# Kernel tuning notes

Measured on AMD Instinct MI355X. Metric: run time of the kernel, lower is better.

Reference implementation:

```python
import jax, jax.numpy as jnp
import numpy as np

N = 50000          # total nodes (types: 20000/17000/13000)
E = 800000         # edges, avg degree 16
NUM_ETYPES = 6
ALPHA = 0.05       # residual-attention blend coefficient
SLOPE = 0.2        # leaky_relu negative slope


def _edge_softmax(e, dst, n):
    # softmax over incoming edges of each destination node; e: [E, H]
    m = jax.ops.segment_max(e, dst, num_segments=n)      # [N, H]
    ex = jnp.exp(e - m[dst])
    s = jax.ops.segment_sum(ex, dst, num_segments=n)     # [N, H]
    return ex / s[dst]


def _gat_layer(h, src, dst, etype, W, We, eemb, al, ar, ae, resW, res_attn, activate):
    n = h.shape[0]
    H, out = al.shape
    feat = (h @ W).reshape(n, H, out)                    # [N, H, out]
    T, edim = eemb.shape
    # edge-type attention term: embedding -> fc_e -> attn_e; only T distinct rows
    et_att = jnp.einsum('thd,hd->th', (eemb @ We).reshape(T, H, edim), ae)  # [T, H]
    el = jnp.einsum('nho,ho->nh', feat, al)              # [N, H]
    er = jnp.einsum('nho,ho->nh', feat, ar)              # [N, H]
    e = jax.nn.leaky_relu(el[src] + er[dst] + et_att[etype], SLOPE)  # [E, H]
    a = _edge_softmax(e, dst, n)                         # [E, H]
    if res_attn is not None:
        a = a * (1.0 - ALPHA) + res_attn * ALPHA
    rst = jax.ops.segment_sum(feat[src] * a[:, :, None], dst, num_segments=n)  # [N, H, out]
    if resW is not None:
        rst = rst + (h @ resW).reshape(n, H, out)
    if activate:
        rst = jax.nn.elu(rst)
    return rst, jax.lax.stop_gradient(a)


def _forward(x0, x1, x2, fcw0, fcb0, fcw1, fcb1, fcw2, fcb2,
             W0, We0, eemb0, al0, ar0, ae0,
             W1, We1, eemb1, al1, ar1, ae1, resW1,
             W2, We2, eemb2, al2, ar2, ae2, resW2,
             src, dst, etype):
    # per-type input projection then concat (feat_drop=0 -> identity)
    h = jnp.concatenate([x0 @ fcw0 + fcb0, x1 @ fcw1 + fcb1, x2 @ fcw2 + fcb2], axis=0)  # [N, 64]
    h1, a = _gat_layer(h, src, dst, etype, W0, We0, eemb0, al0, ar0, ae0, None, None, True)
    h1 = h1.reshape(h1.shape[0], -1)                     # [N, 256]
    h2, a = _gat_layer(h1, src, dst, etype, W1, We1, eemb1, al1, ar1, ae1, resW1, a, True)
    h2 = h2.reshape(h2.shape[0], -1)                     # [N, 256]
    logits, _ = _gat_layer(h2, src, dst, etype, W2, We2, eemb2, al2, ar2, ae2, resW2, None, False)
    return logits                                        # [N, 1, 16]


def setup_inputs():
    key = jax.random.key(0)
    ks = iter(jax.random.split(key, 48))
    def rn(shape, fan_in):
        return jax.random.normal(next(ks), shape, jnp.float32) / np.sqrt(fan_in)
    inp = {}
    inp['x0'] = jax.random.normal(next(ks), (20000, 128), jnp.float32)
    inp['x1'] = jax.random.normal(next(ks), (17000, 256), jnp.float32)
    inp['x2'] = jax.random.normal(next(ks), (13000, 64), jnp.float32)
    inp['fcw0'] = rn((128, 64), 128); inp['fcb0'] = jnp.zeros((64,), jnp.float32)
    inp['fcw1'] = rn((256, 64), 256); inp['fcb1'] = jnp.zeros((64,), jnp.float32)
    inp['fcw2'] = rn((64, 64), 64);   inp['fcb2'] = jnp.zeros((64,), jnp.float32)
    # layer 0: in=64 -> H=8, out=32
    inp['W0'] = rn((64, 256), 64); inp['We0'] = rn((64, 512), 64)
    inp['eemb0'] = rn((NUM_ETYPES, 64), 1.0)
    inp['al0'] = rn((8, 32), 32); inp['ar0'] = rn((8, 32), 32); inp['ae0'] = rn((8, 64), 64)
    # layer 1: in=256 -> H=8, out=32, residual
    inp['W1'] = rn((256, 256), 256); inp['We1'] = rn((64, 512), 64)
    inp['eemb1'] = rn((NUM_ETYPES, 64), 1.0)
    inp['al1'] = rn((8, 32), 32); inp['ar1'] = rn((8, 32), 32); inp['ae1'] = rn((8, 64), 64)
    inp['resW1'] = rn((256, 256), 256)
    # output layer: in=256 -> H=1, out=16, residual
    inp['W2'] = rn((256, 16), 256); inp['We2'] = rn((64, 64), 64)
    inp['eemb2'] = rn((NUM_ETYPES, 64), 1.0)
    inp['al2'] = rn((1, 16), 16); inp['ar2'] = rn((1, 16), 16); inp['ae2'] = rn((1, 64), 64)
    inp['resW2'] = rn((256, 16), 256)
    inp['src'] = jax.random.randint(next(ks), (E,), 0, N)
    inp['dst'] = jax.random.randint(next(ks), (E,), 0, N)
    inp['etype'] = jax.random.randint(next(ks), (E,), 0, NUM_ETYPES)
    return inp


def reference(x0, x1, x2, fcw0, fcb0, fcw1, fcb1, fcw2, fcb2,
              W0, We0, eemb0, al0, ar0, ae0,
              W1, We1, eemb1, al1, ar1, ae1, resW1,
              W2, We2, eemb2, al2, ar2, ae2, resW2,
              src, dst, etype):
    return _forward(x0, x1, x2, fcw0, fcb0, fcw1, fcb1, fcw2, fcb2,
                    W0, We0, eemb0, al0, ar0, ae0,
                    W1, We1, eemb1, al1, ar1, ae1, resW1,
                    W2, We2, eemb2, al2, ar2, ae2, resW2,
                    src, dst, etype)
```

## Files before the change

kernel.cpp:

```cpp
#include <hip/hip_runtime.h>
#include <hip/hip_bf16.h>

#define ALPHA 0.05f
#define SLOPE 0.2f
#define LCAP 128

typedef __attribute__((ext_vector_type(8))) short short8v;
typedef __attribute__((ext_vector_type(8))) unsigned short ushort8v;
typedef __attribute__((ext_vector_type(4))) float floatx4;

__device__ inline ushort f2b(float f) {
    uint u = __float_as_uint(f);
    return (ushort)((u + 0x7fffu + ((u >> 16) & 1u)) >> 16);
}
__device__ inline float b2f(ushort b) { return __uint_as_float(((uint)b) << 16); }

__device__ inline void gload_lds16(const ushort* g, ushort* l) {
    __builtin_amdgcn_global_load_lds(
        (const __attribute__((address_space(1))) uint*)g,
        (__attribute__((address_space(3))) uint*)l, 16, 0, 0);
}


__global__ void hist_kernel(const int* __restrict__ dst, int* __restrict__ counts, int E) {
    int e = blockIdx.x * blockDim.x + threadIdx.x;
    if (e < E) atomicAdd(&counts[dst[e]], 1);
}

__global__ __launch_bounds__(256) void scan_part(const int* __restrict__ counts,
                                                 int* __restrict__ offsets,
                                                 int* __restrict__ partial, int n) {
    __shared__ int sd[256];
    int i = blockIdx.x * 256 + threadIdx.x;
    int v = (i < n) ? counts[i] : 0;
    sd[threadIdx.x] = v;
    __syncthreads();
    for (int off = 1; off < 256; off <<= 1) {
        int t = (threadIdx.x >= off) ? sd[threadIdx.x - off] : 0;
        __syncthreads();
        sd[threadIdx.x] += t;
        __syncthreads();
    }
    if (i < n) offsets[i + 1] = sd[threadIdx.x];
    if (threadIdx.x == 255) partial[blockIdx.x] = sd[255];
}

__global__ __launch_bounds__(256) void scan_top(int* __restrict__ partial, int nb) {
    __shared__ int sd[256];
    int v = (threadIdx.x < nb) ? partial[threadIdx.x] : 0;
    sd[threadIdx.x] = v;
    __syncthreads();
    for (int off = 1; off < 256; off <<= 1) {
        int t = (threadIdx.x >= off) ? sd[threadIdx.x - off] : 0;
        __syncthreads();
        sd[threadIdx.x] += t;
        __syncthreads();
    }
    if (threadIdx.x < nb) partial[threadIdx.x] = sd[threadIdx.x];
}

__global__ __launch_bounds__(256) void scan_add(int* __restrict__ offsets,
                                                int* __restrict__ cursor,
                                                const int* __restrict__ partial, int n) {
    int i = blockIdx.x * 256 + threadIdx.x;
    if (i >= n) return;
    int add = (blockIdx.x > 0) ? partial[blockIdx.x - 1] : 0;
    int v = offsets[i + 1] + add;
    offsets[i + 1] = v;
    if (i + 1 < n) cursor[i + 1] = v;
    if (i == 0) { offsets[0] = 0; cursor[0] = 0; }
}

__global__ void scatter_kernel(const int* __restrict__ src, const int* __restrict__ dst,
                               const int* __restrict__ et, int* __restrict__ cursor,
                               int* __restrict__ se, int E) {
    int e = blockIdx.x * blockDim.x + threadIdx.x;
    if (e >= E) return;
    int d = dst[e];
    int pos = atomicAdd(&cursor[d], 1);
    se[pos] = (src[e] << 3) | et[e];
}


__global__ void wprep(const float* __restrict__ W0f, const float* __restrict__ W1f,
                      const float* __restrict__ WRf,
                      const float* __restrict__ fw0, const float* __restrict__ fw1,
                      const float* __restrict__ fw2,
                      const float* __restrict__ W2f, const float* __restrict__ WR2f,
                      ushort* __restrict__ Wt0, ushort* __restrict__ Wt1,
                      ushort* __restrict__ WtR,
                      ushort* __restrict__ ft0, ushort* __restrict__ ft1,
                      ushort* __restrict__ ft2, ushort* __restrict__ Wt2R) {
    int i = blockIdx.x * blockDim.x + threadIdx.x;
    if (i < 16384) {
        int k = i / 256, n = i % 256;
        Wt0[n * 64 + k] = f2b(W0f[i]);
    } else if (i < 16384 + 65536) {
        int j = i - 16384;
        int k = j / 256, n = j % 256;
        Wt1[n * 256 + k] = f2b(W1f[j]);
    } else if (i < 16384 + 2 * 65536) {
        int j = i - 16384 - 65536;
        int k = j / 256, n = j % 256;
        WtR[n * 256 + k] = f2b(WRf[j]);
    } else if (i < 147456 + 8192) {
        int j = i - 147456;
        int k = j / 64, n = j % 64;
        ft0[n * 128 + k] = f2b(fw0[j]);
    } else if (i < 147456 + 8192 + 16384) {
        int j = i - 147456 - 8192;
        int k = j / 64, n = j % 64;
        ft1[n * 256 + k] = f2b(fw1[j]);
    } else if (i < 147456 + 8192 + 16384 + 4096) {
        int j = i - 147456 - 8192 - 16384;
        int k = j / 64, n = j % 64;
        ft2[n * 64 + k] = f2b(fw2[j]);
    } else if (i < 176128 + 4096) {
        int j = i - 176128;
        int k = j / 16, n = j % 16;
        Wt2R[n * 256 + k] = f2b(W2f[j]);
    } else if (i < 176128 + 8192) {
        int j = i - 176128 - 4096;
        int k = j / 16, n = j % 16;
        Wt2R[(16 + n) * 256 + k] = f2b(WR2f[j]);
    }
}


__global__ __launch_bounds__(512) void etype_all(
    const float* __restrict__ eemb0, const float* __restrict__ We0, const float* __restrict__ ae0, float* __restrict__ out0,
    const float* __restrict__ eemb1, const float* __restrict__ We1, const float* __restrict__ ae1, float* __restrict__ out1,
    const float* __restrict__ eemb2, const float* __restrict__ We2, const float* __restrict__ ae2, float* __restrict__ out2) {
    int layer = blockIdx.x / 6, t = blockIdx.x % 6;
    const float *eemb, *We, *ae;
    float* out;
    int H;
    if (layer == 0)      { eemb = eemb0; We = We0; ae = ae0; out = out0; H = 8; }
    else if (layer == 1) { eemb = eemb1; We = We1; ae = ae1; out = out1; H = 8; }
    else                 { eemb = eemb2; We = We2; ae = ae2; out = out2; H = 1; }
    __shared__ float es[64];
    int j = threadIdx.x;
    if (j < 64) es[j] = eemb[t * 64 + j];
    __syncthreads();
    if (j >= H * 64) return;
    float wsum = 0.f;
#pragma unroll 8
    for (int k = 0; k < 64; ++k) wsum += es[k] * We[k * (H * 64) + j];
    float v = wsum * ae[j];
#pragma unroll
    for (int off = 32; off > 0; off >>= 1) v += __shfl_down(v, off, 64);
    if ((j & 63) == 0) out[t * H + (j >> 6)] = v;
}


template<bool ATTN>
__global__ __launch_bounds__(256) void gemm_bf16(const ushort* __restrict__ A,
                                                 const ushort* __restrict__ Bt,
                                                 ushort* __restrict__ Cb,
                                                 const float* __restrict__ al,
                                                 const float* __restrict__ ar,
                                                 float* __restrict__ el,
                                                 float* __restrict__ er,
                                                 int M, int N, int K) {
    __shared__ ushort As[128 * 32];
    __shared__ ushort Bs[128 * 32];
    int bm = blockIdx.y * 128, bn = blockIdx.x * 128;
    int tid = threadIdx.x;
    int wave = tid >> 6, lane = tid & 63;
    int wm = (wave >> 1) * 64, wn = (wave & 1) * 64;
    int r = tid >> 2, c = (tid & 3) * 8;
    floatx4 acc[4][4] = {};
    for (int k0 = 0; k0 < K; k0 += 32) {
        gload_lds16(&A[(long)(bm + r) * K + k0 + c],       &As[(size_t)tid * 8]);
        gload_lds16(&A[(long)(bm + 64 + r) * K + k0 + c],  &As[(size_t)(256 + tid) * 8]);
        gload_lds16(&Bt[(long)(bn + r) * K + k0 + c],      &Bs[(size_t)tid * 8]);
        gload_lds16(&Bt[(long)(bn + 64 + r) * K + k0 + c], &Bs[(size_t)(256 + tid) * 8]);
        __syncthreads();
        int lr = lane & 15, lk = (lane >> 4) * 8;
        short8v af[4], bfr[4];
#pragma unroll
        for (int i = 0; i < 4; ++i)
            af[i] = *reinterpret_cast<const short8v*>(&As[(wm + i * 16 + lr) * 32 + lk]);
#pragma unroll
        for (int j = 0; j < 4; ++j)
            bfr[j] = *reinterpret_cast<const short8v*>(&Bs[(wn + j * 16 + lr) * 32 + lk]);
#pragma unroll
        for (int i = 0; i < 4; ++i)
#pragma unroll
            for (int j = 0; j < 4; ++j)
                acc[i][j] = __builtin_amdgcn_mfma_f32_16x16x32_bf16(af[i], bfr[j], acc[i][j], 0, 0, 0);
        __syncthreads();
    }
    int col = lane & 15, rbase = (lane >> 4) * 4;
#pragma unroll
    for (int i = 0; i < 4; ++i) {
#pragma unroll
        for (int rr = 0; rr < 4; ++rr) {
            int gm = bm + wm + i * 16 + rbase + rr;
            if (gm >= M) continue;
#pragma unroll
            for (int j = 0; j < 4; ++j) {
                int gn = bn + wn + j * 16 + col;
                Cb[(long)gm * N + gn] = f2b(acc[i][j][rr]);
            }
        }
    }
    if (ATTN) {
        int hA = (bn + wn) >> 5;
        float alv[4], arv[4];
#pragma unroll
        for (int j = 0; j < 4; ++j) {
            int h = hA + (j >> 1);
            int o = (j & 1) * 16 + col;
            alv[j] = al[h * 32 + o];
            arv[j] = ar[h * 32 + o];
        }
#pragma unroll
        for (int i = 0; i < 4; ++i) {
#pragma unroll
            for (int rr = 0; rr < 4; ++rr) {
                float slA = acc[i][0][rr] * alv[0] + acc[i][1][rr] * alv[1];
                float slB = acc[i][2][rr] * alv[2] + acc[i][3][rr] * alv[3];
                float srA = acc[i][0][rr] * arv[0] + acc[i][1][rr] * arv[1];
                float srB = acc[i][2][rr] * arv[2] + acc[i][3][rr] * arv[3];
#pragma unroll
                for (int off = 1; off < 16; off <<= 1) {
                    slA += __shfl_xor(slA, off, 64);
                    slB += __shfl_xor(slB, off, 64);
                    srA += __shfl_xor(srA, off, 64);
                    srB += __shfl_xor(srB, off, 64);
                }
                int gm = bm + wm + i * 16 + rbase + rr;
                if (col == 0 && gm < M) {
                    el[gm * 8 + hA]     = slA;
                    el[gm * 8 + hA + 1] = slB;
                    er[gm * 8 + hA]     = srA;
                    er[gm * 8 + hA + 1] = srB;
                }
            }
        }
    }
}


__global__ __launch_bounds__(256) void gemm_dual(const ushort* __restrict__ A,
                                                 const ushort* __restrict__ B1,
                                                 const ushort* __restrict__ B2,
                                                 ushort* __restrict__ C1,
                                                 ushort* __restrict__ C2,
                                                 const float* __restrict__ al,
                                                 const float* __restrict__ ar,
                                                 float* __restrict__ el,
                                                 float* __restrict__ er,
                                                 int M, int N, int K) {
    __shared__ ushort As[128 * 32];
    __shared__ ushort Bs1[128 * 32];
    __shared__ ushort Bs2[128 * 32];
    int bm = blockIdx.y * 128, bn = blockIdx.x * 128;
    int tid = threadIdx.x;
    int wave = tid >> 6, lane = tid & 63;
    int wm = (wave >> 1) * 64, wn = (wave & 1) * 64;
    int r = tid >> 2, c = (tid & 3) * 8;
    floatx4 acc1[4][4] = {};
    floatx4 acc2[4][4] = {};
    for (int k0 = 0; k0 < K; k0 += 32) {
        gload_lds16(&A[(long)(bm + r) * K + k0 + c],        &As[(size_t)tid * 8]);
        gload_lds16(&A[(long)(bm + 64 + r) * K + k0 + c],   &As[(size_t)(256 + tid) * 8]);
        gload_lds16(&B1[(long)(bn + r) * K + k0 + c],       &Bs1[(size_t)tid * 8]);
        gload_lds16(&B1[(long)(bn + 64 + r) * K + k0 + c],  &Bs1[(size_t)(256 + tid) * 8]);
        gload_lds16(&B2[(long)(bn + r) * K + k0 + c],       &Bs2[(size_t)tid * 8]);
        gload_lds16(&B2[(long)(bn + 64 + r) * K + k0 + c],  &Bs2[(size_t)(256 + tid) * 8]);
        __syncthreads();
        int lr = lane & 15, lk = (lane >> 4) * 8;
        short8v af[4], bfr[4];
#pragma unroll
        for (int i = 0; i < 4; ++i)
            af[i] = *reinterpret_cast<const short8v*>(&As[(wm + i * 16 + lr) * 32 + lk]);
#pragma unroll
        for (int j = 0; j < 4; ++j)
            bfr[j] = *reinterpret_cast<const short8v*>(&Bs1[(wn + j * 16 + lr) * 32 + lk]);
#pragma unroll
        for (int i = 0; i < 4; ++i)
#pragma unroll
            for (int j = 0; j < 4; ++j)
                acc1[i][j] = __builtin_amdgcn_mfma_f32_16x16x32_bf16(af[i], bfr[j], acc1[i][j], 0, 0, 0);
#pragma unroll
        for (int j = 0; j < 4; ++j)
            bfr[j] = *reinterpret_cast<const short8v*>(&Bs2[(wn + j * 16 + lr) * 32 + lk]);
#pragma unroll
        for (int i = 0; i < 4; ++i)
#pragma unroll
            for (int j = 0; j < 4; ++j)
                acc2[i][j] = __builtin_amdgcn_mfma_f32_16x16x32_bf16(af[i], bfr[j], acc2[i][j], 0, 0, 0);
        __syncthreads();
    }
    int col = lane & 15, rbase = (lane >> 4) * 4;
#pragma unroll
    for (int i = 0; i < 4; ++i) {
#pragma unroll
        for (int rr = 0; rr < 4; ++rr) {
            int gm = bm + wm + i * 16 + rbase + rr;
            if (gm >= M) continue;
#pragma unroll
            for (int j = 0; j < 4; ++j) {
                int gn = bn + wn + j * 16 + col;
                C1[(long)gm * N + gn] = f2b(acc1[i][j][rr]);
                C2[(long)gm * N + gn] = f2b(acc2[i][j][rr]);
            }
        }
    }
    int hA = (bn + wn) >> 5;
    float alv[4], arv[4];
#pragma unroll
    for (int j = 0; j < 4; ++j) {
        int h = hA + (j >> 1);
        int o = (j & 1) * 16 + col;
        alv[j] = al[h * 32 + o];
        arv[j] = ar[h * 32 + o];
    }
#pragma unroll
    for (int i = 0; i < 4; ++i) {
#pragma unroll
        for (int rr = 0; rr < 4; ++rr) {
            float slA = acc1[i][0][rr] * alv[0] + acc1[i][1][rr] * alv[1];
            float slB = acc1[i][2][rr] * alv[2] + acc1[i][3][rr] * alv[3];
            float srA = acc1[i][0][rr] * arv[0] + acc1[i][1][rr] * arv[1];
            float srB = acc1[i][2][rr] * arv[2] + acc1[i][3][rr] * arv[3];
#pragma unroll
            for (int off = 1; off < 16; off <<= 1) {
                slA += __shfl_xor(slA, off, 64);
                slB += __shfl_xor(slB, off, 64);
                srA += __shfl_xor(srA, off, 64);
                srB += __shfl_xor(srB, off, 64);
            }
            int gm = bm + wm + i * 16 + rbase + rr;
            if (col == 0 && gm < M) {
                el[gm * 8 + hA]     = slA;
                el[gm * 8 + hA + 1] = slB;
                er[gm * 8 + hA]     = srA;
                er[gm * 8 + hA + 1] = srB;
            }
        }
    }
}


__global__ __launch_bounds__(256) void gemm_fc(const float* __restrict__ x0,
                                               const float* __restrict__ x1,
                                               const float* __restrict__ x2,
                                               const ushort* __restrict__ ft0,
                                               const ushort* __restrict__ ft1,
                                               const ushort* __restrict__ ft2,
                                               const float* __restrict__ b0,
                                               const float* __restrict__ b1,
                                               const float* __restrict__ b2,
                                               ushort* __restrict__ C,
                                               int n0, int n1, int n2) {
    int z = blockIdx.z;
    const float* A;
    const ushort* Bt;
    const float* bias;
    int M, K;
    long coff;
    if (z == 0)      { A = x0; Bt = ft0; bias = b0; M = n0; K = 128; coff = 0; }
    else if (z == 1) { A = x1; Bt = ft1; bias = b1; M = n1; K = 256; coff = (long)n0 * 64; }
    else             { A = x2; Bt = ft2; bias = b2; M = n2; K = 64;  coff = (long)(n0 + n1) * 64; }
    int bm = blockIdx.y * 128;
    if (bm >= M) return;
    __shared__ ushort As[128 * 32];
    __shared__ ushort Bs[64 * 32];
    int tid = threadIdx.x;
    int wave = tid >> 6, lane = tid & 63;
    int wm = (wave >> 1) * 64, wn = (wave & 1) * 32;
    int r = tid >> 2, c = (tid & 3) * 8;
    floatx4 acc[4][2] = {};
    for (int k0 = 0; k0 < K; k0 += 32) {
        {
            int gm0 = bm + r, gm1 = bm + 64 + r;
            ushort8v u0 = {0, 0, 0, 0, 0, 0, 0, 0};
            ushort8v u1 = {0, 0, 0, 0, 0, 0, 0, 0};
            if (gm0 < M) {
                float4 lo = *reinterpret_cast<const float4*>(&A[(long)gm0 * K + k0 + c]);
                float4 hi = *reinterpret_cast<const float4*>(&A[(long)gm0 * K + k0 + c + 4]);
                u0[0] = f2b(lo.x); u0[1] = f2b(lo.y); u0[2] = f2b(lo.z); u0[3] = f2b(lo.w);
                u0[4] = f2b(hi.x); u0[5] = f2b(hi.y); u0[6] = f2b(hi.z); u0[7] = f2b(hi.w);
            }
            if (gm1 < M) {
                float4 lo = *reinterpret_cast<const float4*>(&A[(long)gm1 * K + k0 + c]);
                float4 hi = *reinterpret_cast<const float4*>(&A[(long)gm1 * K + k0 + c + 4]);
                u1[0] = f2b(lo.x); u1[1] = f2b(lo.y); u1[2] = f2b(lo.z); u1[3] = f2b(lo.w);
                u1[4] = f2b(hi.x); u1[5] = f2b(hi.y); u1[6] = f2b(hi.z); u1[7] = f2b(hi.w);
            }
            *reinterpret_cast<ushort8v*>(&As[(size_t)tid * 8]) = u0;
            *reinterpret_cast<ushort8v*>(&As[(size_t)(256 + tid) * 8]) = u1;
        }
        gload_lds16(&Bt[(long)r * K + k0 + c], &Bs[(size_t)tid * 8]);
        __syncthreads();
        int lr = lane & 15, lk = (lane >> 4) * 8;
        short8v af[4], bfr[2];
#pragma unroll
        for (int i = 0; i < 4; ++i)
            af[i] = *reinterpret_cast<const short8v*>(&As[(wm + i * 16 + lr) * 32 + lk]);
#pragma unroll
        for (int j = 0; j < 2; ++j)
            bfr[j] = *reinterpret_cast<const short8v*>(&Bs[(wn + j * 16 + lr) * 32 + lk]);
#pragma unroll
        for (int i = 0; i < 4; ++i)
#pragma unroll
            for (int j = 0; j < 2; ++j)
                acc[i][j] = __builtin_amdgcn_mfma_f32_16x16x32_bf16(af[i], bfr[j], acc[i][j], 0, 0, 0);
        __syncthreads();
    }
    int col = lane & 15, rbase = (lane >> 4) * 4;
#pragma unroll
    for (int i = 0; i < 4; ++i) {
#pragma unroll
        for (int rr = 0; rr < 4; ++rr) {
            int gm = bm + wm + i * 16 + rbase + rr;
            if (gm >= M) continue;
#pragma unroll
            for (int j = 0; j < 2; ++j) {
                int gn = wn + j * 16 + col;
                C[coff + (long)gm * 64 + gn] = f2b(acc[i][j][rr] + bias[gn]);
            }
        }
    }
}


__global__ __launch_bounds__(256) void gemm_small(const ushort* __restrict__ A,
                                                  const ushort* __restrict__ Wt2R,
                                                  ushort* __restrict__ feat2b,
                                                  float* __restrict__ resout,
                                                  const float* __restrict__ al,
                                                  const float* __restrict__ ar,
                                                  float* __restrict__ el,
                                                  float* __restrict__ er, int M) {
    __shared__ ushort As[128 * 32];
    __shared__ ushort Bs[32 * 256];
    int tid = threadIdx.x;
    int wave = tid >> 6, lane = tid & 63;
    int bm = blockIdx.x * 128;
    for (int i = tid; i < 32 * 256 / 8; i += 256)
        *reinterpret_cast<ushort8v*>(&Bs[(size_t)i * 8]) =
            *reinterpret_cast<const ushort8v*>(&Wt2R[(size_t)i * 8]);
    __syncthreads();
    int r = tid >> 2, c = (tid & 3) * 8;
    floatx4 acc[2][2] = {};
    for (int k0 = 0; k0 < 256; k0 += 32) {
        gload_lds16(&A[(long)(bm + r) * 256 + k0 + c],      &As[(size_t)tid * 8]);
        gload_lds16(&A[(long)(bm + 64 + r) * 256 + k0 + c], &As[(size_t)(256 + tid) * 8]);
        __syncthreads();
        int lr = lane & 15, lk = (lane >> 4) * 8;
        short8v af[2], bfr[2];
#pragma unroll
        for (int i = 0; i < 2; ++i)
            af[i] = *reinterpret_cast<const short8v*>(&As[(wave * 32 + i * 16 + lr) * 32 + lk]);
#pragma unroll
        for (int j = 0; j < 2; ++j)
            bfr[j] = *reinterpret_cast<const short8v*>(&Bs[(j * 16 + lr) * 256 + k0 + lk]);
#pragma unroll
        for (int i = 0; i < 2; ++i)
#pragma unroll
            for (int j = 0; j < 2; ++j)
                acc[i][j] = __builtin_amdgcn_mfma_f32_16x16x32_bf16(af[i], bfr[j], acc[i][j], 0, 0, 0);
        __syncthreads();
    }
    int col = lane & 15, rbase = (lane >> 4) * 4;
    float alv = al[col], arv = ar[col];
#pragma unroll
    for (int i = 0; i < 2; ++i) {
#pragma unroll
        for (int rr = 0; rr < 4; ++rr) {
            int gm = bm + wave * 32 + i * 16 + rbase + rr;
            float s1 = acc[i][0][rr];
            float s2 = acc[i][1][rr];
            float sl = s1 * alv, sr = s1 * arv;
#pragma unroll
            for (int off = 1; off < 16; off <<= 1) {
                sl += __shfl_xor(sl, off, 64);
                sr += __shfl_xor(sr, off, 64);
            }
            if (gm < M) {
                feat2b[(long)gm * 16 + col] = f2b(s1);
                resout[(long)gm * 16 + col] = s2;
                if (col == 0) { el[gm] = sl; er[gm] = sr; }
            }
        }
    }
}


template<bool BLEND, bool SAVE, bool RES>
__global__ __launch_bounds__(64) void fused_edge_h8(
    const int* __restrict__ offsets, const int* __restrict__ se,
    const float* __restrict__ el, const float* __restrict__ er,
    const float* __restrict__ etatt,
    const ushort* __restrict__ featb,
    const ushort* __restrict__ a0_in, ushort* __restrict__ a0_out,
    const ushort* __restrict__ resin, ushort* __restrict__ outb, int N) {
    int d = blockIdx.x;
    int lane = threadIdx.x;
    int lo = offsets[d], hi = offsets[d + 1];
    int deg = hi - lo;
    __shared__ float a_lds[LCAP][8];
    __shared__ int   s_lds[LCAP];
    __shared__ float er_s[8];
    __shared__ float m_s[8], inv_s[8];
    if (lane < 8) er_s[lane] = er[d * 8 + lane];
    __syncthreads();
    bool fast = (deg <= LCAP);
    int half = lane >> 5, t = lane & 31;
    int h8 = t >> 2;
    uint4 pf[4];
    int npf = 0;
    if (fast) {
        for (int i = lane; i < deg * 8; i += 64) {
            int p = i >> 3, h = i & 7;
            int v0 = se[lo + p];
            int s = v0 >> 3, tt = v0 & 7;
            if (h == 0) s_lds[p] = s;
            float v = el[s * 8 + h] + er_s[h] + etatt[tt * 8 + h];
            a_lds[p][h] = v > 0.f ? v : SLOPE * v;
        }
        __syncthreads();
#pragma unroll
        for (int u = 0; u < 4; ++u) {
            int p = half + 2 * u;
            if (p < deg) {
                pf[u] = *reinterpret_cast<const uint4*>(&featb[(long)s_lds[p] * 256 + t * 8]);
                npf = u + 1;
            }
        }
        {
            int g = lane >> 3, h = lane & 7;
            float m = -INFINITY;
            for (int p = g; p < deg; p += 8) m = fmaxf(m, a_lds[p][h]);
#pragma unroll
            for (int off = 8; off < 64; off <<= 1) m = fmaxf(m, __shfl_xor(m, off, 64));
            float ssum = 0.f;
            for (int p = g; p < deg; p += 8) ssum += __expf(a_lds[p][h] - m);
#pragma unroll
            for (int off = 8; off < 64; off <<= 1) ssum += __shfl_xor(ssum, off, 64);
            if (g == 0) {
                m_s[h] = m;
                inv_s[h] = ssum > 0.f ? 1.f / ssum : 0.f;
            }
        }
        __syncthreads();
        for (int i = lane; i < deg * 8; i += 64) {
            int p = i >> 3, h = i & 7;
            float a = __expf(a_lds[p][h] - m_s[h]) * inv_s[h];
            if (BLEND) a = a * (1.f - ALPHA) + b2f(a0_in[lo * 8 + i]) * ALPHA;
            a_lds[p][h] = a;
            if (SAVE) a0_out[lo * 8 + i] = f2b(a);
        }
        __syncthreads();
    } else {
        int g = lane >> 3, h = lane & 7;
        float m = -INFINITY;
        for (int p = g; p < deg; p += 8) {
            int v0 = se[lo + p];
            int s = v0 >> 3, tt = v0 & 7;
            float v = el[s * 8 + h] + er_s[h] + etatt[tt * 8 + h];
            v = v > 0.f ? v : SLOPE * v;
            m = fmaxf(m, v);
        }
#pragma unroll
        for (int off = 8; off < 64; off <<= 1) m = fmaxf(m, __shfl_xor(m, off, 64));
        float ssum = 0.f;
        for (int p = g; p < deg; p += 8) {
            int v0 = se[lo + p];
            int s = v0 >> 3, tt = v0 & 7;
            float v = el[s * 8 + h] + er_s[h] + etatt[tt * 8 + h];
            v = v > 0.f ? v : SLOPE * v;
            ssum += __expf(v - m);
        }
#pragma unroll
        for (int off = 8; off < 64; off <<= 1) ssum += __shfl_xor(ssum, off, 64);
        if (g == 0) {
            m_s[h] = m;
            inv_s[h] = ssum > 0.f ? 1.f / ssum : 0.f;
        }
        __syncthreads();
        if (SAVE) {
            for (int i = lane; i < deg * 8; i += 64) {
                int p = i >> 3, hh = i & 7;
                int v0 = se[lo + p];
                int s = v0 >> 3, tt = v0 & 7;
                float v = el[s * 8 + hh] + er_s[hh] + etatt[tt * 8 + hh];
                v = v > 0.f ? v : SLOPE * v;
                float a = __expf(v - m_s[hh]) * inv_s[hh];
                if (BLEND) a = a * (1.f - ALPHA) + b2f(a0_in[lo * 8 + i]) * ALPHA;
                a0_out[lo * 8 + i] = f2b(a);
            }
        }
    }
    float acc[8];
#pragma unroll
    for (int k = 0; k < 8; ++k) acc[k] = 0.f;
    if (RES && half == 0) {
        uint4 rv = *reinterpret_cast<const uint4*>(&resin[(long)d * 256 + t * 8]);
        const uint* rp = reinterpret_cast<const uint*>(&rv);
#pragma unroll
        for (int q = 0; q < 4; ++q) {
            acc[2 * q]     = __uint_as_float(rp[q] << 16);
            acc[2 * q + 1] = __uint_as_float(rp[q] & 0xffff0000u);
        }
    }
    if (fast) {
#pragma unroll
        for (int u = 0; u < 4; ++u) {
            if (u < npf) {
                float a = a_lds[half + 2 * u][h8];
                const uint* fp = reinterpret_cast<const uint*>(&pf[u]);
#pragma unroll
                for (int q = 0; q < 4; ++q) {
                    acc[2 * q]     += __uint_as_float(fp[q] << 16) * a;
                    acc[2 * q + 1] += __uint_as_float(fp[q] & 0xffff0000u) * a;
                }
            }
        }
        int p = half + 8;
        for (; p + 6 < deg; p += 8) {
            int s0 = s_lds[p],     s1 = s_lds[p + 2];
            int s2 = s_lds[p + 4], s3 = s_lds[p + 6];
            float a0 = a_lds[p][h8],     a1 = a_lds[p + 2][h8];
            float a2 = a_lds[p + 4][h8], a3 = a_lds[p + 6][h8];
            uint4 f0 = *reinterpret_cast<const uint4*>(&featb[(long)s0 * 256 + t * 8]);
            uint4 f1 = *reinterpret_cast<const uint4*>(&featb[(long)s1 * 256 + t * 8]);
            uint4 f2 = *reinterpret_cast<const uint4*>(&featb[(long)s2 * 256 + t * 8]);
            uint4 f3 = *reinterpret_cast<const uint4*>(&featb[(long)s3 * 256 + t * 8]);
            const uint* q0 = reinterpret_cast<const uint*>(&f0);
            const uint* q1 = reinterpret_cast<const uint*>(&f1);
            const uint* q2 = reinterpret_cast<const uint*>(&f2);
            const uint* q3 = reinterpret_cast<const uint*>(&f3);
#pragma unroll
            for (int q = 0; q < 4; ++q) {
                acc[2 * q] += __uint_as_float(q0[q] << 16) * a0
                            + __uint_as_float(q1[q] << 16) * a1
                            + __uint_as_float(q2[q] << 16) * a2
                            + __uint_as_float(q3[q] << 16) * a3;
                acc[2 * q + 1] += __uint_as_float(q0[q] & 0xffff0000u) * a0
                                + __uint_as_float(q1[q] & 0xffff0000u) * a1
                                + __uint_as_float(q2[q] & 0xffff0000u) * a2
                                + __uint_as_float(q3[q] & 0xffff0000u) * a3;
            }
        }
        for (; p < deg; p += 2) {
            int s = s_lds[p];
            float a = a_lds[p][h8];
            uint4 fv = *reinterpret_cast<const uint4*>(&featb[(long)s * 256 + t * 8]);
            const uint* fp = reinterpret_cast<const uint*>(&fv);
#pragma unroll
            for (int q = 0; q < 4; ++q) {
                uint u = fp[q];
                acc[2 * q]     += __uint_as_float(u << 16) * a;
                acc[2 * q + 1] += __uint_as_float(u & 0xffff0000u) * a;
            }
        }
    } else {
        for (int p = half; p < deg; p += 2) {
            int v0 = se[lo + p];
            int s = v0 >> 3, tt = v0 & 7;
            float v = el[s * 8 + h8] + er_s[h8] + etatt[tt * 8 + h8];
            v = v > 0.f ? v : SLOPE * v;
            float a = __expf(v - m_s[h8]) * inv_s[h8];
            if (BLEND) a = a * (1.f - ALPHA) + b2f(a0_in[(long)(lo + p) * 8 + h8]) * ALPHA;
            uint4 fv = *reinterpret_cast<const uint4*>(&featb[(long)s * 256 + t * 8]);
            const uint* fp = reinterpret_cast<const uint*>(&fv);
#pragma unroll
            for (int q = 0; q < 4; ++q) {
                uint u = fp[q];
                acc[2 * q]     += __uint_as_float(u << 16) * a;
                acc[2 * q + 1] += __uint_as_float(u & 0xffff0000u) * a;
            }
        }
    }
#pragma unroll
    for (int k = 0; k < 8; ++k) acc[k] += __shfl_down(acc[k], 32);
    if (half == 0) {
        ushort8v o;
#pragma unroll
        for (int k = 0; k < 8; ++k) {
            float v = acc[k];
            v = v > 0.f ? v : __expf(v) - 1.f;
            o[k] = f2b(v);
        }
        *reinterpret_cast<ushort8v*>(&outb[(long)d * 256 + t * 8]) = o;
    }
}


__global__ __launch_bounds__(64) void fused_edge_h1(
    const int* __restrict__ offsets, const int* __restrict__ se,
    const float* __restrict__ el, const float* __restrict__ er,
    const float* __restrict__ etatt,
    const ushort* __restrict__ featb2, const float* __restrict__ resout,
    float* __restrict__ out, int N) {
    int d = blockIdx.x;
    int lane = threadIdx.x;
    int lo = offsets[d], hi = offsets[d + 1];
    int deg = hi - lo;
    __shared__ float a_lds[512];
    float er_d = er[d];
    bool fast = (deg <= 512);
    float m = -INFINITY, inv = 0.f;
    if (fast) {
        for (int i = lane; i < deg; i += 64) {
            int v0 = se[lo + i];
            int s = v0 >> 3, t = v0 & 7;
            float v = el[s] + er_d + etatt[t];
            a_lds[i] = v > 0.f ? v : SLOPE * v;
        }
        __syncthreads();
        for (int i = lane; i < deg; i += 64) m = fmaxf(m, a_lds[i]);
#pragma unroll
        for (int off = 1; off < 64; off <<= 1) m = fmaxf(m, __shfl_xor(m, off, 64));
        float ssum = 0.f;
        for (int i = lane; i < deg; i += 64) ssum += __expf(a_lds[i] - m);
#pragma unroll
        for (int off = 1; off < 64; off <<= 1) ssum += __shfl_xor(ssum, off, 64);
        inv = ssum > 0.f ? 1.f / ssum : 0.f;
        for (int i = lane; i < deg; i += 64) a_lds[i] = __expf(a_lds[i] - m) * inv;
        __syncthreads();
    } else {
        for (int i = lane; i < deg; i += 64) {
            int v0 = se[lo + i];
            int s = v0 >> 3, t = v0 & 7;
            float v = el[s] + er_d + etatt[t];
            v = v > 0.f ? v : SLOPE * v;
            m = fmaxf(m, v);
        }
#pragma unroll
        for (int off = 1; off < 64; off <<= 1) m = fmaxf(m, __shfl_xor(m, off, 64));
        float ssum = 0.f;
        for (int i = lane; i < deg; i += 64) {
            int v0 = se[lo + i];
            int s = v0 >> 3, t = v0 & 7;
            float v = el[s] + er_d + etatt[t];
            v = v > 0.f ? v : SLOPE * v;
            ssum += __expf(v - m);
        }
#pragma unroll
        for (int off = 1; off < 64; off <<= 1) ssum += __shfl_xor(ssum, off, 64);
        inv = ssum > 0.f ? 1.f / ssum : 0.f;
    }
    int g = lane >> 1, t = lane & 1;
    float acc[8];
#pragma unroll
    for (int k = 0; k < 8; ++k) acc[k] = 0.f;
    for (int p = g; p < deg; p += 32) {
        int v0 = se[lo + p];
        int s = v0 >> 3;
        float a;
        if (fast) a = a_lds[p];
        else {
            int tt = v0 & 7;
            float v = el[s] + er_d + etatt[tt];
            v = v > 0.f ? v : SLOPE * v;
            a = __expf(v - m) * inv;
        }
        uint4 fv = *reinterpret_cast<const uint4*>(&featb2[(long)s * 16 + t * 8]);
        const uint* fp = reinterpret_cast<const uint*>(&fv);
#pragma unroll
        for (int q = 0; q < 4; ++q) {
            acc[2 * q]     += __uint_as_float(fp[q] << 16) * a;
            acc[2 * q + 1] += __uint_as_float(fp[q] & 0xffff0000u) * a;
        }
    }
#pragma unroll
    for (int off = 2; off < 64; off <<= 1)
#pragma unroll
        for (int k = 0; k < 8; ++k) acc[k] += __shfl_down(acc[k], off);
    if (lane < 2) {
        const float* rp = &resout[(long)d * 16 + t * 8];
        float4 r0 = *reinterpret_cast<const float4*>(rp);
        float4 r1 = *reinterpret_cast<const float4*>(rp + 4);
        float* op = &out[(long)d * 16 + t * 8];
        *reinterpret_cast<float4*>(op)     = make_float4(acc[0] + r0.x, acc[1] + r0.y, acc[2] + r0.z, acc[3] + r0.w);
        *reinterpret_cast<float4*>(op + 4) = make_float4(acc[4] + r1.x, acc[5] + r1.y, acc[6] + r1.z, acc[7] + r1.w);
    }
}


extern "C" void kernel_launch(void* const* d_in, const int* in_sizes, int n_in,
                              void* d_out, int out_size, void* d_ws, size_t ws_size,
                              hipStream_t stream) {
    const float* x0   = (const float*)d_in[0];
    const float* x1   = (const float*)d_in[1];
    const float* x2   = (const float*)d_in[2];
    const float* fcw0 = (const float*)d_in[3];
    const float* fcb0 = (const float*)d_in[4];
    const float* fcw1 = (const float*)d_in[5];
    const float* fcb1 = (const float*)d_in[6];
    const float* fcw2 = (const float*)d_in[7];
    const float* fcb2 = (const float*)d_in[8];
    const float* W0   = (const float*)d_in[9];
    const float* We0  = (const float*)d_in[10];
    const float* eemb0= (const float*)d_in[11];
    const float* al0  = (const float*)d_in[12];
    const float* ar0  = (const float*)d_in[13];
    const float* ae0  = (const float*)d_in[14];
    const float* W1   = (const float*)d_in[15];
    const float* We1  = (const float*)d_in[16];
    const float* eemb1= (const float*)d_in[17];
    const float* al1  = (const float*)d_in[18];
    const float* ar1  = (const float*)d_in[19];
    const float* ae1  = (const float*)d_in[20];
    const float* resW1= (const float*)d_in[21];
    const float* W2   = (const float*)d_in[22];
    const float* We2  = (const float*)d_in[23];
    const float* eemb2= (const float*)d_in[24];
    const float* al2  = (const float*)d_in[25];
    const float* ar2  = (const float*)d_in[26];
    const float* ae2  = (const float*)d_in[27];
    const float* resW2= (const float*)d_in[28];
    const int* src    = (const int*)d_in[29];
    const int* dst    = (const int*)d_in[30];
    const int* etype  = (const int*)d_in[31];

    const int n0 = in_sizes[0] / 128;
    const int n1 = in_sizes[1] / 256;
    const int n2 = in_sizes[2] / 64;
    const int N  = n0 + n1 + n2;
    const int E  = in_sizes[29];

    char* w = (char*)d_ws;
    auto alloc = [&](size_t bytes) {
        char* p = w;
        w += (bytes + 255) & ~(size_t)255;
        return p;
    };
    int*    counts  = (int*)alloc((size_t)N * 4);
    int*    offsets = (int*)alloc((size_t)(N + 1) * 4);
    int*    cursor  = (int*)alloc((size_t)N * 4);
    int*    partial = (int*)alloc(1024 * 4);
    int*    se      = (int*)alloc((size_t)E * 4);
    ushort* h2res   = (ushort*)alloc((size_t)N * 256 * 2);
    ushort* a0b     = (ushort*)alloc((size_t)E * 8 * 2);
    ushort* h0bf    = (ushort*)alloc((size_t)N * 64 * 2 + 128 * 256 * 2);
    ushort* featb   = (ushort*)alloc((size_t)N * 256 * 2);
    ushort* h1bf    = (ushort*)alloc((size_t)N * 256 * 2 + 128 * 256 * 2);
    ushort* h2bf    = (ushort*)alloc((size_t)N * 256 * 2 + 128 * 256 * 2);
    float*  el      = (float*)alloc((size_t)N * 8 * 4);
    float*  er      = (float*)alloc((size_t)N * 8 * 4);
    float*  etatt0  = (float*)alloc(64 * 4);
    float*  etatt1  = (float*)alloc(64 * 4);
    float*  etatt2  = (float*)alloc(64 * 4);
    ushort* Wt0     = (ushort*)alloc((size_t)256 * 64 * 2);
    ushort* Wt1     = (ushort*)alloc((size_t)256 * 256 * 2);
    ushort* WtR     = (ushort*)alloc((size_t)256 * 256 * 2);
    ushort* ft0     = (ushort*)alloc((size_t)64 * 128 * 2);
    ushort* ft1     = (ushort*)alloc((size_t)64 * 256 * 2);
    ushort* ft2     = (ushort*)alloc((size_t)64 * 64 * 2);
    ushort* Wt2R    = (ushort*)alloc((size_t)32 * 256 * 2);
    ushort* feat2b  = (ushort*)alloc((size_t)N * 16 * 2);
    float*  resout  = (float*)alloc((size_t)N * 16 * 4);
    float*  out     = (float*)d_out;

    const int TB = 256;
    int eb = (E + TB - 1) / TB;
    int nb1 = (N + 255) / 256;

    hipMemsetAsync(counts, 0, (size_t)N * 4, stream);
    hist_kernel<<<eb, TB, 0, stream>>>(dst, counts, E);
    scan_part<<<nb1, 256, 0, stream>>>(counts, offsets, partial, N);
    scan_top<<<1, 256, 0, stream>>>(partial, nb1);
    scan_add<<<nb1, 256, 0, stream>>>(offsets, cursor, partial, N);
    scatter_kernel<<<eb, TB, 0, stream>>>(src, dst, etype, cursor, se, E);

    wprep<<<(184320 + TB - 1) / TB, TB, 0, stream>>>(W0, W1, resW1, fcw0, fcw1, fcw2,
                                                     W2, resW2,
                                                     Wt0, Wt1, WtR, ft0, ft1, ft2, Wt2R);
    etype_all<<<18, 512, 0, stream>>>(eemb0, We0, ae0, etatt0,
                                      eemb1, We1, ae1, etatt1,
                                      eemb2, We2, ae2, etatt2);

    {
        int maxM = n0 > n1 ? n0 : n1;
        if (n2 > maxM) maxM = n2;
        dim3 g(1, (maxM + 127) / 128, 3);
        gemm_fc<<<g, TB, 0, stream>>>(x0, x1, x2, ft0, ft1, ft2, fcb0, fcb1, fcb2,
                                      h0bf, n0, n1, n2);
    }

    dim3 gg(256 / 128, (N + 127) / 128);

    gemm_bf16<true><<<gg, TB, 0, stream>>>(h0bf, Wt0, featb, al0, ar0, el, er, N, 256, 64);
    fused_edge_h8<false, true, false><<<N, 64, 0, stream>>>(
        offsets, se, el, er, etatt0, featb, nullptr, a0b, nullptr, h1bf, N);

    gemm_dual<<<gg, TB, 0, stream>>>(h1bf, Wt1, WtR, featb, h2res, al1, ar1, el, er, N, 256, 256);
    fused_edge_h8<true, false, true><<<N, 64, 0, stream>>>(
        offsets, se, el, er, etatt1, featb, a0b, nullptr, h2res, h2bf, N);

    gemm_small<<<(N + 127) / 128, TB, 0, stream>>>(
        h2bf, Wt2R, feat2b, resout, al2, ar2, el, er, N);
    fused_edge_h1<<<N, 64, 0, stream>>>(offsets, se, el, er, etatt2, feat2b, resout, out, N);
}
```

Measured before the change: 394.9 us.

## Stage gathered feature rows through LDS with double-buffered async loads

```diff
diff --git a/kernel.cpp b/kernel.cpp
--- a/kernel.cpp
+++ b/kernel.cpp
@@ -3,7 +3,7 @@
 
 #define ALPHA 0.05f
 #define SLOPE 0.2f
-#define LCAP 128
+#define LCAP 64
 
 typedef __attribute__((ext_vector_type(8))) short short8v;
 typedef __attribute__((ext_vector_type(8))) unsigned short ushort8v;
@@ -507,13 +507,12 @@
     __shared__ int   s_lds[LCAP];
     __shared__ float er_s[8];
     __shared__ float m_s[8], inv_s[8];
+    __shared__ ushort stage[2][2048];
     if (lane < 8) er_s[lane] = er[d * 8 + lane];
     __syncthreads();
     bool fast = (deg <= LCAP);
     int half = lane >> 5, t = lane & 31;
     int h8 = t >> 2;
-    uint4 pf[4];
-    int npf = 0;
     if (fast) {
         for (int i = lane; i < deg * 8; i += 64) {
             int p = i >> 3, h = i & 7;
@@ -524,14 +523,6 @@
             a_lds[p][h] = v > 0.f ? v : SLOPE * v;
         }
         __syncthreads();
-#pragma unroll
-        for (int u = 0; u < 4; ++u) {
-            int p = half + 2 * u;
-            if (p < deg) {
-                pf[u] = *reinterpret_cast<const uint4*>(&featb[(long)s_lds[p] * 256 + t * 8]);
-                npf = u + 1;
-            }
-        }
         {
             int g = lane >> 3, h = lane & 7;
             float m = -INFINITY;
@@ -609,55 +600,43 @@
         }
     }
     if (fast) {
-#pragma unroll
-        for (int u = 0; u < 4; ++u) {
-            if (u < npf) {
-                float a = a_lds[half + 2 * u][h8];
-                const uint* fp = reinterpret_cast<const uint*>(&pf[u]);
-#pragma unroll
-                for (int q = 0; q < 4; ++q) {
-                    acc[2 * q]     += __uint_as_float(fp[q] << 16) * a;
-                    acc[2 * q + 1] += __uint_as_float(fp[q] & 0xffff0000u) * a;
+        auto issue = [&](int buf, int pb) {
+#pragma unroll
+            for (int u = 0; u < 4; ++u) {
+                int e0 = pb + 2 * u, e1 = pb + 2 * u + 1;
+                e0 = e0 < deg ? e0 : deg - 1;
+                e1 = e1 < deg ? e1 : deg - 1;
+                int srow = (lane < 32) ? s_lds[e0] : s_lds[e1];
+                gload_lds16(&featb[(long)srow * 256 + (lane & 31) * 8],
+                            &stage[buf][u * 512]);
+            }
+        };
+        issue(0, 0);
+        if (deg > 8) issue(1, 8);
+        for (int pb = 0; pb < deg; pb += 8) {
+            int cur = (pb >> 3) & 1;
+            if (pb + 8 < deg) {
+                asm volatile("s_waitcnt vmcnt(4)" ::: "memory");
+            } else {
+                asm volatile("s_waitcnt vmcnt(0)" ::: "memory");
+            }
+            __builtin_amdgcn_sched_barrier(0);
+#pragma unroll
+            for (int u = 0; u < 4; ++u) {
+                int j = half * 4 + u;
+                if (pb + j < deg) {
+                    float a = a_lds[pb + j][h8];
+                    uint4 fv = *reinterpret_cast<const uint4*>(&stage[cur][j * 256 + t * 8]);
+                    const uint* fp = reinterpret_cast<const uint*>(&fv);
+#pragma unroll
+                    for (int q = 0; q < 4; ++q) {
+                        acc[2 * q]     += __uint_as_float(fp[q] << 16) * a;
+                        acc[2 * q + 1] += __uint_as_float(fp[q] & 0xffff0000u) * a;
+                    }
                 }
             }
-        }
-        int p = half + 8;
-        for (; p + 6 < deg; p += 8) {
-            int s0 = s_lds[p],     s1 = s_lds[p + 2];
-            int s2 = s_lds[p + 4], s3 = s_lds[p + 6];
-            float a0 = a_lds[p][h8],     a1 = a_lds[p + 2][h8];
-            float a2 = a_lds[p + 4][h8], a3 = a_lds[p + 6][h8];
-            uint4 f0 = *reinterpret_cast<const uint4*>(&featb[(long)s0 * 256 + t * 8]);
-            uint4 f1 = *reinterpret_cast<const uint4*>(&featb[(long)s1 * 256 + t * 8]);
-            uint4 f2 = *reinterpret_cast<const uint4*>(&featb[(long)s2 * 256 + t * 8]);
-            uint4 f3 = *reinterpret_cast<const uint4*>(&featb[(long)s3 * 256 + t * 8]);
-            const uint* q0 = reinterpret_cast<const uint*>(&f0);
-            const uint* q1 = reinterpret_cast<const uint*>(&f1);
-            const uint* q2 = reinterpret_cast<const uint*>(&f2);
-            const uint* q3 = reinterpret_cast<const uint*>(&f3);
-#pragma unroll
-            for (int q = 0; q < 4; ++q) {
-                acc[2 * q] += __uint_as_float(q0[q] << 16) * a0
-                            + __uint_as_float(q1[q] << 16) * a1
-                            + __uint_as_float(q2[q] << 16) * a2
-                            + __uint_as_float(q3[q] << 16) * a3;
-                acc[2 * q + 1] += __uint_as_float(q0[q] & 0xffff0000u) * a0
-                                + __uint_as_float(q1[q] & 0xffff0000u) * a1
-                                + __uint_as_float(q2[q] & 0xffff0000u) * a2
-                                + __uint_as_float(q3[q] & 0xffff0000u) * a3;
-            }
-        }
-        for (; p < deg; p += 2) {
-            int s = s_lds[p];
-            float a = a_lds[p][h8];
-            uint4 fv = *reinterpret_cast<const uint4*>(&featb[(long)s * 256 + t * 8]);
-            const uint* fp = reinterpret_cast<const uint*>(&fv);
-#pragma unroll
-            for (int q = 0; q < 4; ++q) {
-                uint u = fp[q];
-                acc[2 * q]     += __uint_as_float(u << 16) * a;
-                acc[2 * q + 1] += __uint_as_float(u & 0xffff0000u) * a;
-            }
+            __builtin_amdgcn_sched_barrier(0);
+            if (pb + 16 < deg) issue(cur, pb + 16);
         }
     } else {
         for (int p = half; p < deg; p += 2) {
```

New measurement: 446.9 us. 13.2% more time.
